# Optimization experiments

Hardware: AMD Instinct MI355X
Metric: run time of the kernel (lower is better)

Reference implementation:

```python
import jax, jax.numpy as jnp
import numpy as np

EPS = 1e-4

def mp_weight(w):
    # MP_GeoLinear eval-mode weight: normalize then scale by gain/sqrt(fan_in)
    w32 = w.astype(jnp.float32)
    norm = jnp.linalg.norm(w32, axis=1, keepdims=True)          # [out,1]
    fan_in = w.shape[1]
    denom = EPS + norm / np.sqrt(fan_in)                        # torch.add(eps, norm, alpha=sqrt(1/fan_in))
    wn = w32 / denom
    return (wn / np.sqrt(fan_in)).astype(w.dtype)               # gain=1


def setup_inputs() -> dict:
    key = jax.random.key(0)
    k1, k2, k3, k4 = jax.random.split(key, 4)
    N, E, C = 100000, 1600000, 128
    x = jax.random.normal(k1, (N, C), dtype=jnp.float32)
    edge_index = jax.random.randint(k2, (2, E), 0, N, dtype=jnp.int64)
    w_neigh = jax.random.normal(k3, (C, C), dtype=jnp.float32)
    w_res = jax.random.normal(k4, (C, C), dtype=jnp.float32)
    return {"x": x, "edge_index": edge_index, "w_neigh": w_neigh, "w_res": w_res}


def reference(x, edge_index, w_neigh, w_res):
    N = x.shape[0]
    row, col = edge_index[0], edge_index[1]            # source, target
    # degree of target nodes
    deg = jax.ops.segment_sum(jnp.ones_like(col, dtype=x.dtype), col, num_segments=N)
    deg_inv = jnp.where(deg > 0, deg ** -0.5, 0.0)     # inf -> 0
    norm = deg_inv[col]                                 # [E]
    # message: x_j * norm, aggregate: scatter-add into col
    msg = x[row] * norm[:, None]                        # [E,C]
    agg = jax.ops.segment_sum(msg, col, num_segments=N) # [N,C]
    neighbourhood = agg @ mp_weight(w_neigh).T
    residual = x @ mp_weight(w_res).T
    # mp_sum(residual, neighbourhood, t=0.5) = (a+b)/sqrt(2)
    join = (residual + neighbourhood) / np.sqrt(2.0)
    out = jnp.where((deg > 0)[:, None], join, residual)
    return out
```

## Files before the change

### kernel.cpp

```cpp
#include <hip/hip_runtime.h>
#include <hip/hip_bf16.h>

#define C 128
#define INV_SQRT2 0.7071067811865476f
#define NB 1024
#define BS 128
#define EPB 4096
#define NXCD 8
#define SUBCAP 384
#define LIDX_CAP 4096
#define AGS 68

typedef __attribute__((ext_vector_type(8))) short short8;
typedef __attribute__((ext_vector_type(4))) float f32x4;

__device__ inline ushort f2b(float f) {
    __hip_bfloat16 h = __float2bfloat16(f);
    return __builtin_bit_cast(ushort, h);
}


__global__ __launch_bounds__(512) void k_front(
    const int* __restrict__ row, const int* __restrict__ col, int E, int nblk,
    int* __restrict__ gcursor, unsigned int* __restrict__ recs,
    const float4* __restrict__ x, ushort* __restrict__ xb, int n4, int castBlocks,
    const float* __restrict__ w_res, const float* __restrict__ w_neigh,
    ushort* __restrict__ Bp)
{
    __shared__ int hist[NB];
    __shared__ int lbase[NB];
    int b = blockIdx.x;
    int t = threadIdx.x;
    if (b < nblk) {
        hist[t] = 0; hist[t + 512] = 0;
        __syncthreads();
        int base = b * EPB;
        #pragma unroll
        for (int i = 0; i < EPB / 512; i++) {
            int e = base + i * 512 + t;
            if (e < E) atomicAdd(&hist[col[e] >> 7], 1);
        }
        __syncthreads();
        int xcd = b & 7;
        int* gc = gcursor + xcd * NB;
        #pragma unroll
        for (int kx = 0; kx < 2; kx++) {
            int bb = t + kx * 512;
            int h = hist[bb];
            lbase[bb] = h ? atomicAdd(&gc[bb], h) : 0;
        }
        __syncthreads();
        hist[t] = 0; hist[t + 512] = 0;
        __syncthreads();
        #pragma unroll
        for (int i = 0; i < EPB / 512; i++) {
            int e = base + i * 512 + t;
            if (e < E) {
                int c = col[e];
                int kk = c >> 7;
                int p = atomicAdd(&hist[kk], 1) + lbase[kk];
                if (p < SUBCAP)
                    recs[((size_t)kk * NXCD + xcd) * SUBCAP + p] =
                        ((unsigned int)(c & 127) << 24) | (unsigned int)row[e];
            }
        }
    } else if (b < nblk + castBlocks) {
        int i = (b - nblk) * 512 + t;
        if (i < n4) {
            float4 v = x[i];
            ushort4 o;
            o.x = f2b(v.x); o.y = f2b(v.y); o.z = f2b(v.z); o.w = f2b(v.w);
            *(ushort4*)(xb + (size_t)i * 4) = o;
        }
        if (b == nblk && t < 32) {
            ushort4 z = make_ushort4(0, 0, 0, 0);
            *(ushort4*)(xb + ((size_t)n4 << 2) + (t << 2)) = z;
        }
    } else {
        int r = (b - nblk - castBlocks) * 8 + (t >> 6);
        int h = r >> 7;
        int i = r & 127;
        const float* w = h ? w_neigh : w_res;
        int lane = t & 63;
        float a = w[i * C + lane];
        float bb = w[i * C + lane + 64];
        float ss = a * a + bb * bb;
        #pragma unroll
        for (int off = 32; off > 0; off >>= 1) ss += __shfl_down(ss, off);
        ss = __shfl(ss, 0);
        float norm = sqrtf(ss);
        float denom = 1e-4f + norm * 0.08838834764831845f;
        float scale = 1.0f / (denom * 11.313708498984761f);
        int c1 = lane, c2 = lane + 64;
        Bp[(size_t)(h * 16 + (c1 >> 3)) * 1024 + i * 8 + (c1 & 7)] = f2b(a * scale);
        Bp[(size_t)(h * 16 + (c2 >> 3)) * 1024 + i * 8 + (c2 & 7)] = f2b(bb * scale);
    }
}


#define ACCUM(v) do { \
    acc[0] += __builtin_bit_cast(float, (v).x << 16); \
    acc[1] += __builtin_bit_cast(float, (v).x & 0xffff0000u); \
    acc[2] += __builtin_bit_cast(float, (v).y << 16); \
    acc[3] += __builtin_bit_cast(float, (v).y & 0xffff0000u); \
    acc[4] += __builtin_bit_cast(float, (v).z << 16); \
    acc[5] += __builtin_bit_cast(float, (v).z & 0xffff0000u); \
    acc[6] += __builtin_bit_cast(float, (v).w << 16); \
    acc[7] += __builtin_bit_cast(float, (v).w & 0xffff0000u); \
} while (0)

__global__ __launch_bounds__(512, 8) void k_fused(
    const unsigned int* __restrict__ recs, const int* __restrict__ gcursor,
    const ushort* __restrict__ xb, const ushort* __restrict__ Bp,
    int* __restrict__ lidxg, float* __restrict__ out, int N)
{
    __shared__ int shist[BS];
    __shared__ int sexcl[BS];
    __shared__ int scur[BS];
    __shared__ int scnt[NXCD];
    __shared__ uint sAgg[BS * AGS];

    int k = blockIdx.x;
    int t = threadIdx.x;
    const unsigned int* rb = recs + (size_t)k * NXCD * SUBCAP;
    int* lw = lidxg + (size_t)k * LIDX_CAP;

    if (t < NXCD) {
        int c = gcursor[t * NB + k];
        scnt[t] = (c > SUBCAP) ? SUBCAP : c;
    }
    if (t < BS) shist[t] = 0;
    __syncthreads();
    #pragma unroll 1
    for (int x = 0; x < NXCD; x++) {
        int cx = scnt[x];
        for (int i = t; i < cx; i += 512)
            atomicAdd(&shist[rb[x * SUBCAP + i] >> 24], 1);
    }
    __syncthreads();
    if (t < 64) {
        int a = shist[t], b = shist[t + 64];
        int pa = (a + 7) & ~7, pb = (b + 7) & ~7;
        int ia = pa, ib = pb;
        #pragma unroll
        for (int off = 1; off < 64; off <<= 1) {
            int ya = __shfl_up(ia, off);
            int yb = __shfl_up(ib, off);
            if (t >= off) { ia += ya; ib += yb; }
        }
        int tot0 = __shfl(ia, 63);
        int e0 = ia - pa;
        int e1 = ib - pb + tot0;
        sexcl[t] = e0;      scur[t] = e0;
        sexcl[t + 64] = e1; scur[t + 64] = e1;
    }
    __syncthreads();
    #pragma unroll 1
    for (int x = 0; x < NXCD; x++) {
        int cx = scnt[x];
        for (int i = t; i < cx; i += 512) {
            unsigned int r = rb[x * SUBCAP + i];
            int c = r >> 24;
            int p = atomicAdd(&scur[c], 1);
            lw[p] = (int)(r & 0xFFFFFF);
        }
    }
    if (t < BS) {
        int d = shist[t], b0 = sexcl[t];
        int pe = b0 + ((d + 7) & ~7);
        for (int p = b0 + d; p < pe; p++) lw[p] = N;
    }
    __syncthreads();

    int lane = t & 63;
    int wave = t >> 6;
    int s  = lane >> 4;
    int cl = lane & 15;
    const ushort* xcl = xb + (cl << 3);
    #pragma unroll 1
    for (int ln = wave * 16; ln < wave * 16 + 16; ln++) {
        int j  = sexcl[ln];
        int d  = shist[ln];
        int jend = j + ((d + 7) & ~7);
        float acc[8];
        #pragma unroll
        for (int i = 0; i < 8; i++) acc[i] = 0.f;
        for (; j + 16 <= jend; j += 16) {
            int i0 = lw[j + s];
            int i1 = lw[j + 4 + s];
            int i2 = lw[j + 8 + s];
            int i3 = lw[j + 12 + s];
            uint4 va = *(const uint4*)(xcl + ((size_t)i0 << 7));
            uint4 vb = *(const uint4*)(xcl + ((size_t)i1 << 7));
            uint4 vc = *(const uint4*)(xcl + ((size_t)i2 << 7));
            uint4 vd = *(const uint4*)(xcl + ((size_t)i3 << 7));
            ACCUM(va);
            ACCUM(vb);
            ACCUM(vc);
            ACCUM(vd);
        }
        if (j < jend) {
            int i0 = lw[j + s];
            int i1 = lw[j + 4 + s];
            uint4 va = *(const uint4*)(xcl + ((size_t)i0 << 7));
            uint4 vb = *(const uint4*)(xcl + ((size_t)i1 << 7));
            ACCUM(va);
            ACCUM(vb);
        }
        #pragma unroll
        for (int i = 0; i < 8; i++) {
            acc[i] += __shfl_xor(acc[i], 16);
            acc[i] += __shfl_xor(acc[i], 32);
        }
        float dd = (d > 0) ? rsqrtf((float)d) : 0.f;
        if (lane < 16) {
            uint4 o;
            o.x = (uint)f2b(acc[0] * dd) | ((uint)f2b(acc[1] * dd) << 16);
            o.y = (uint)f2b(acc[2] * dd) | ((uint)f2b(acc[3] * dd) << 16);
            o.z = (uint)f2b(acc[4] * dd) | ((uint)f2b(acc[5] * dd) << 16);
            o.w = (uint)f2b(acc[6] * dd) | ((uint)f2b(acc[7] * dd) << 16);
            *(uint4*)&sAgg[ln * AGS + cl * 4] = o;
        }
    }
    asm volatile("s_waitcnt lgkmcnt(0)" ::: "memory");

    int quad = lane >> 4;
    int l16  = lane & 15;
    long gbase = (long)k * BS;
    int arow = wave * 16 + l16;
    long garow = gbase + arow;
    if (garow >= N) garow = N - 1;

    f32x4 oacc[8];
    #pragma unroll
    for (int nt = 0; nt < 8; nt++) oacc[nt] = (f32x4){0.f, 0.f, 0.f, 0.f};

    #pragma unroll
    for (int kk = 0; kk < 8; kk++) {
        short8 af;
        if (kk < 4) {
            af = *(const short8*)(xb + garow * C + kk * 32 + quad * 8);
        } else {
            af = *(const short8*)&sAgg[arow * AGS + (kk - 4) * 16 + quad * 4];
        }
        #pragma unroll
        for (int nt = 0; nt < 8; nt++) {
            short8 bf = *(const short8*)(Bp +
                ((size_t)((kk * 4 + quad) * 128) + nt * 16 + l16) * 8);
            oacc[nt] = __builtin_amdgcn_mfma_f32_16x16x32_bf16(af, bf, oacc[nt], 0, 0, 0);
        }
    }

    #pragma unroll
    for (int r2 = 0; r2 < 4; r2++) {
        int rl = wave * 16 + quad * 4 + r2;
        long rowg = gbase + rl;
        if (rowg < N) {
            float sc = (shist[rl] > 0) ? INV_SQRT2 : 1.0f;
            float* o = out + rowg * C + l16;
            #pragma unroll
            for (int nt = 0; nt < 8; nt++)
                __builtin_nontemporal_store(oacc[nt][r2] * sc, &o[nt * 16]);
        }
    }
}


extern "C" void kernel_launch(void* const* d_in, const int* in_sizes, int n_in,
                              void* d_out, int out_size, void* d_ws, size_t ws_size,
                              hipStream_t stream) {
    const float* x       = (const float*)d_in[0];
    const int*   eidx    = (const int*)d_in[1];
    const float* w_neigh = (const float*)d_in[2];
    const float* w_res   = (const float*)d_in[3];
    float* out = (float*)d_out;

    int N = in_sizes[0] / C;
    int E = in_sizes[1] / 2;
    const int* row = eidx;
    const int* col = eidx + E;

    char* ws = (char*)d_ws;
    size_t off = 0;
    auto alloc = [&](size_t bytes) {
        size_t o = off;
        off += (bytes + 511) & ~(size_t)511;
        return o;
    };
    int nblk = (E + EPB - 1) / EPB;

    int*    gcursor    = (int*)(ws + alloc((size_t)NXCD * NB * 4));
    unsigned int* recs = (unsigned int*)(ws + alloc((size_t)NB * NXCD * SUBCAP * 4));
    ushort* Bp         = (ushort*)(ws + alloc((size_t)32 * 1024 * 2));
    ushort* xb         = (ushort*)(ws + alloc((size_t)N * C * 2 + 65536));
    int*    lidxg      = (int*)(ws + alloc((size_t)NB * LIDX_CAP * 4));
    (void)ws_size;

    hipMemsetAsync(gcursor, 0, (size_t)NXCD * NB * 4, stream);

    int nbuckets = (N + BS - 1) / BS;
    int n4 = N * C / 4;
    int castBlocks = (n4 + 511) / 512;

    k_front<<<nblk + castBlocks + 32, 512, 0, stream>>>(
        row, col, E, nblk, gcursor, recs,
        (const float4*)x, xb, n4, castBlocks, w_res, w_neigh, Bp);
    k_fused<<<nbuckets, 512, 0, stream>>>(recs, gcursor, xb, Bp, lidxg, out, N);
}
```

Before: 210.9 us.

## Merge front and fused kernels into one persistent cooperative kernel with grid sync

Replaces the two-kernel pipeline (bucketing/cast/weight prep, then aggregation+MFMA) with a single cooperative persistent kernel of up to 768 blocks. The blocks loop over the bucketing and weight work, cast x to bf16 through a dynamic atomic work counter, wait at a grid-wide barrier, then loop over the node buckets. This removes a kernel launch boundary and tail effects, but adds the grid sync cost and caps parallelism at the persistent grid size. It falls back to the old two-kernel path if the cooperative launch fails.

```diff
diff --git a/kernel.cpp b/kernel.cpp
--- a/kernel.cpp
+++ b/kernel.cpp
@@ -1,5 +1,8 @@
 #include <hip/hip_runtime.h>
 #include <hip/hip_bf16.h>
+#include <hip/hip_cooperative_groups.h>
+
+namespace cg = cooperative_groups;
 
 #define C 128
 #define INV_SQRT2 0.7071067811865476f
@@ -10,6 +13,7 @@
 #define SUBCAP 384
 #define LIDX_CAP 4096
 #define AGS 68
+#define COOP_GRID 768
 
 typedef __attribute__((ext_vector_type(8))) short short8;
 typedef __attribute__((ext_vector_type(4))) float f32x4;
@@ -17,6 +21,270 @@
 __device__ inline ushort f2b(float f) {
     __hip_bfloat16 h = __float2bfloat16(f);
     return __builtin_bit_cast(ushort, h);
+}
+
+#define ACCUM(v) do { \
+    acc[0] += __builtin_bit_cast(float, (v).x << 16); \
+    acc[1] += __builtin_bit_cast(float, (v).x & 0xffff0000u); \
+    acc[2] += __builtin_bit_cast(float, (v).y << 16); \
+    acc[3] += __builtin_bit_cast(float, (v).y & 0xffff0000u); \
+    acc[4] += __builtin_bit_cast(float, (v).z << 16); \
+    acc[5] += __builtin_bit_cast(float, (v).z & 0xffff0000u); \
+    acc[6] += __builtin_bit_cast(float, (v).w << 16); \
+    acc[7] += __builtin_bit_cast(float, (v).w & 0xffff0000u); \
+} while (0)
+
+
+__global__ __launch_bounds__(512, 8) void k_all(
+    const int* __restrict__ row, const int* __restrict__ col, int E, int nblk,
+    int* __restrict__ gcursor, unsigned int* __restrict__ recs,
+    const float4* __restrict__ x, ushort* __restrict__ xb, int n4,
+    int* __restrict__ castcur,
+    const float* __restrict__ w_res, const float* __restrict__ w_neigh,
+    ushort* __restrict__ Bp, int* __restrict__ lidxg,
+    float* __restrict__ out, int N)
+{
+    __shared__ uint sAgg[BS * AGS];
+    __shared__ int shist[BS];
+    __shared__ int sexcl[BS];
+    __shared__ int scur[BS];
+    __shared__ int scnt8[NXCD];
+    __shared__ int swork;
+
+    int b = blockIdx.x;
+    int t = threadIdx.x;
+    int gdim = gridDim.x;
+    int lane = t & 63;
+    int wave = t >> 6;
+    int nbuckets = (N + BS - 1) / BS;
+
+    for (int it = b; it < nblk + 32; it += gdim) {
+        __syncthreads();
+        if (it < nblk) {
+            int* hist  = (int*)sAgg;
+            int* lbase = (int*)sAgg + NB;
+            hist[t] = 0; hist[t + 512] = 0;
+            __syncthreads();
+            int base = it * EPB;
+            #pragma unroll
+            for (int i = 0; i < EPB / 512; i++) {
+                int e = base + i * 512 + t;
+                if (e < E) atomicAdd(&hist[col[e] >> 7], 1);
+            }
+            __syncthreads();
+            int xcd = it & 7;
+            int* gc = gcursor + xcd * NB;
+            #pragma unroll
+            for (int kx = 0; kx < 2; kx++) {
+                int bb = t + kx * 512;
+                int h = hist[bb];
+                lbase[bb] = h ? atomicAdd(&gc[bb], h) : 0;
+            }
+            __syncthreads();
+            hist[t] = 0; hist[t + 512] = 0;
+            __syncthreads();
+            #pragma unroll
+            for (int i = 0; i < EPB / 512; i++) {
+                int e = base + i * 512 + t;
+                if (e < E) {
+                    int c = col[e];
+                    int kk = c >> 7;
+                    int p = atomicAdd(&hist[kk], 1) + lbase[kk];
+                    if (p < SUBCAP)
+                        recs[((size_t)kk * NXCD + xcd) * SUBCAP + p] =
+                            ((unsigned int)(c & 127) << 24) | (unsigned int)row[e];
+                }
+            }
+        } else {
+            int r = (it - nblk) * 8 + wave;
+            int h = r >> 7;
+            int i = r & 127;
+            const float* w = h ? w_neigh : w_res;
+            float a = w[i * C + lane];
+            float bb = w[i * C + lane + 64];
+            float ss = a * a + bb * bb;
+            #pragma unroll
+            for (int off = 32; off > 0; off >>= 1) ss += __shfl_down(ss, off);
+            ss = __shfl(ss, 0);
+            float norm = sqrtf(ss);
+            float denom = 1e-4f + norm * 0.08838834764831845f;
+            float scale = 1.0f / (denom * 11.313708498984761f);
+            int c1 = lane, c2 = lane + 64;
+            Bp[(size_t)(h * 16 + (c1 >> 3)) * 1024 + i * 8 + (c1 & 7)] = f2b(a * scale);
+            Bp[(size_t)(h * 16 + (c2 >> 3)) * 1024 + i * 8 + (c2 & 7)] = f2b(bb * scale);
+        }
+    }
+    if (b == 0 && t < 32) {
+        ushort4 z = make_ushort4(0, 0, 0, 0);
+        *(ushort4*)(xb + ((size_t)n4 << 2) + (t << 2)) = z;
+    }
+
+    int nchunk = (n4 + 4095) >> 12;
+    for (;;) {
+        __syncthreads();
+        if (t == 0) swork = atomicAdd(castcur, 1);
+        __syncthreads();
+        int cc = swork;
+        if (cc >= nchunk) break;
+        int i0 = (cc << 12) + t;
+        #pragma unroll
+        for (int u = 0; u < 8; u++) {
+            int i = i0 + (u << 9);
+            if (i < n4) {
+                float4 v = x[i];
+                ushort4 o;
+                o.x = f2b(v.x); o.y = f2b(v.y); o.z = f2b(v.z); o.w = f2b(v.w);
+                *(ushort4*)(xb + (size_t)i * 4) = o;
+            }
+        }
+    }
+
+    __threadfence();
+    cg::this_grid().sync();
+    __threadfence();
+
+    for (int k = b; k < nbuckets; k += gdim) {
+        __syncthreads();
+        const unsigned int* rb = recs + (size_t)k * NXCD * SUBCAP;
+        int* lw = lidxg + (size_t)k * LIDX_CAP;
+
+        if (t < NXCD) {
+            int c0 = gcursor[t * NB + k];
+            scnt8[t] = (c0 > SUBCAP) ? SUBCAP : c0;
+        }
+        if (t < BS) shist[t] = 0;
+        __syncthreads();
+        #pragma unroll 1
+        for (int xx = 0; xx < NXCD; xx++) {
+            int cx = scnt8[xx];
+            for (int i = t; i < cx; i += 512)
+                atomicAdd(&shist[rb[xx * SUBCAP + i] >> 24], 1);
+        }
+        __syncthreads();
+        if (t < 64) {
+            int a = shist[t], bb = shist[t + 64];
+            int pa = (a + 7) & ~7, pb = (bb + 7) & ~7;
+            int ia = pa, ib = pb;
+            #pragma unroll
+            for (int off = 1; off < 64; off <<= 1) {
+                int ya = __shfl_up(ia, off);
+                int yb = __shfl_up(ib, off);
+                if (t >= off) { ia += ya; ib += yb; }
+            }
+            int tot0 = __shfl(ia, 63);
+            int e0 = ia - pa;
+            int e1 = ib - pb + tot0;
+            sexcl[t] = e0;      scur[t] = e0;
+            sexcl[t + 64] = e1; scur[t + 64] = e1;
+        }
+        __syncthreads();
+        #pragma unroll 1
+        for (int xx = 0; xx < NXCD; xx++) {
+            int cx = scnt8[xx];
+            for (int i = t; i < cx; i += 512) {
+                unsigned int r = rb[xx * SUBCAP + i];
+                int c = r >> 24;
+                int p = atomicAdd(&scur[c], 1);
+                lw[p] = (int)(r & 0xFFFFFF);
+            }
+        }
+        if (t < BS) {
+            int d = shist[t], b0 = sexcl[t];
+            int pe = b0 + ((d + 7) & ~7);
+            for (int p = b0 + d; p < pe; p++) lw[p] = N;
+        }
+        __syncthreads();
+
+        int s  = lane >> 4;
+        int cl = lane & 15;
+        const ushort* xcl = xb + (cl << 3);
+        #pragma unroll 1
+        for (int ln = wave * 16; ln < wave * 16 + 16; ln++) {
+            int j  = sexcl[ln];
+            int d  = shist[ln];
+            int jend = j + ((d + 7) & ~7);
+            float acc[8];
+            #pragma unroll
+            for (int i = 0; i < 8; i++) acc[i] = 0.f;
+            for (; j + 16 <= jend; j += 16) {
+                int i0 = lw[j + s];
+                int i1 = lw[j + 4 + s];
+                int i2 = lw[j + 8 + s];
+                int i3 = lw[j + 12 + s];
+                uint4 va = *(const uint4*)(xcl + ((size_t)i0 << 7));
+                uint4 vb = *(const uint4*)(xcl + ((size_t)i1 << 7));
+                uint4 vc = *(const uint4*)(xcl + ((size_t)i2 << 7));
+                uint4 vd = *(const uint4*)(xcl + ((size_t)i3 << 7));
+                ACCUM(va);
+                ACCUM(vb);
+                ACCUM(vc);
+                ACCUM(vd);
+            }
+            if (j < jend) {
+                int i0 = lw[j + s];
+                int i1 = lw[j + 4 + s];
+                uint4 va = *(const uint4*)(xcl + ((size_t)i0 << 7));
+                uint4 vb = *(const uint4*)(xcl + ((size_t)i1 << 7));
+                ACCUM(va);
+                ACCUM(vb);
+            }
+            #pragma unroll
+            for (int i = 0; i < 8; i++) {
+                acc[i] += __shfl_xor(acc[i], 16);
+                acc[i] += __shfl_xor(acc[i], 32);
+            }
+            float dd = (d > 0) ? rsqrtf((float)d) : 0.f;
+            if (lane < 16) {
+                uint4 o;
+                o.x = (uint)f2b(acc[0] * dd) | ((uint)f2b(acc[1] * dd) << 16);
+                o.y = (uint)f2b(acc[2] * dd) | ((uint)f2b(acc[3] * dd) << 16);
+                o.z = (uint)f2b(acc[4] * dd) | ((uint)f2b(acc[5] * dd) << 16);
+                o.w = (uint)f2b(acc[6] * dd) | ((uint)f2b(acc[7] * dd) << 16);
+                *(uint4*)&sAgg[ln * AGS + cl * 4] = o;
+            }
+        }
+        asm volatile("s_waitcnt lgkmcnt(0)" ::: "memory");
+
+        int quad = lane >> 4;
+        int l16  = lane & 15;
+        long gbase = (long)k * BS;
+        int arow = wave * 16 + l16;
+        long garow = gbase + arow;
+        if (garow >= N) garow = N - 1;
+
+        f32x4 oacc[8];
+        #pragma unroll
+        for (int nt = 0; nt < 8; nt++) oacc[nt] = (f32x4){0.f, 0.f, 0.f, 0.f};
+
+        #pragma unroll
+        for (int kk = 0; kk < 8; kk++) {
+            short8 af;
+            if (kk < 4) {
+                af = *(const short8*)(xb + garow * C + kk * 32 + quad * 8);
+            } else {
+                af = *(const short8*)&sAgg[arow * AGS + (kk - 4) * 16 + quad * 4];
+            }
+            #pragma unroll
+            for (int nt = 0; nt < 8; nt++) {
+                short8 bf = *(const short8*)(Bp +
+                    ((size_t)((kk * 4 + quad) * 128) + nt * 16 + l16) * 8);
+                oacc[nt] = __builtin_amdgcn_mfma_f32_16x16x32_bf16(af, bf, oacc[nt], 0, 0, 0);
+            }
+        }
+
+        #pragma unroll
+        for (int r2 = 0; r2 < 4; r2++) {
+            int rl = wave * 16 + quad * 4 + r2;
+            long rowg = gbase + rl;
+            if (rowg < N) {
+                float sc = (shist[rl] > 0) ? INV_SQRT2 : 1.0f;
+                float* o = out + rowg * C + l16;
+                #pragma unroll
+                for (int nt = 0; nt < 8; nt++)
+                    __builtin_nontemporal_store(oacc[nt][r2] * sc, &o[nt * 16]);
+            }
+        }
+    }
 }
 
 
@@ -97,18 +365,6 @@
     }
 }
 
-
-#define ACCUM(v) do { \
-    acc[0] += __builtin_bit_cast(float, (v).x << 16); \
-    acc[1] += __builtin_bit_cast(float, (v).x & 0xffff0000u); \
-    acc[2] += __builtin_bit_cast(float, (v).y << 16); \
-    acc[3] += __builtin_bit_cast(float, (v).y & 0xffff0000u); \
-    acc[4] += __builtin_bit_cast(float, (v).z << 16); \
-    acc[5] += __builtin_bit_cast(float, (v).z & 0xffff0000u); \
-    acc[6] += __builtin_bit_cast(float, (v).w << 16); \
-    acc[7] += __builtin_bit_cast(float, (v).w & 0xffff0000u); \
-} while (0)
-
 __global__ __launch_bounds__(512, 8) void k_fused(
     const unsigned int* __restrict__ recs, const int* __restrict__ gcursor,
     const ushort* __restrict__ xb, const ushort* __restrict__ Bp,
@@ -117,7 +373,7 @@
     __shared__ int shist[BS];
     __shared__ int sexcl[BS];
     __shared__ int scur[BS];
-    __shared__ int scnt[NXCD];
+    __shared__ int scnt8[NXCD];
     __shared__ uint sAgg[BS * AGS];
 
     int k = blockIdx.x;
@@ -126,21 +382,21 @@
     int* lw = lidxg + (size_t)k * LIDX_CAP;
 
     if (t < NXCD) {
-        int c = gcursor[t * NB + k];
-        scnt[t] = (c > SUBCAP) ? SUBCAP : c;
+        int c0 = gcursor[t * NB + k];
+        scnt8[t] = (c0 > SUBCAP) ? SUBCAP : c0;
     }
     if (t < BS) shist[t] = 0;
     __syncthreads();
     #pragma unroll 1
-    for (int x = 0; x < NXCD; x++) {
-        int cx = scnt[x];
+    for (int xx = 0; xx < NXCD; xx++) {
+        int cx = scnt8[xx];
         for (int i = t; i < cx; i += 512)
-            atomicAdd(&shist[rb[x * SUBCAP + i] >> 24], 1);
+            atomicAdd(&shist[rb[xx * SUBCAP + i] >> 24], 1);
     }
     __syncthreads();
     if (t < 64) {
-        int a = shist[t], b = shist[t + 64];
-        int pa = (a + 7) & ~7, pb = (b + 7) & ~7;
+        int a = shist[t], bb = shist[t + 64];
+        int pa = (a + 7) & ~7, pb = (bb + 7) & ~7;
         int ia = pa, ib = pb;
         #pragma unroll
         for (int off = 1; off < 64; off <<= 1) {
@@ -156,10 +412,10 @@
     }
     __syncthreads();
     #pragma unroll 1
-    for (int x = 0; x < NXCD; x++) {
-        int cx = scnt[x];
+    for (int xx = 0; xx < NXCD; xx++) {
+        int cx = scnt8[xx];
         for (int i = t; i < cx; i += 512) {
-            unsigned int r = rb[x * SUBCAP + i];
+            unsigned int r = rb[xx * SUBCAP + i];
             int c = r >> 24;
             int p = atomicAdd(&scur[c], 1);
             lw[p] = (int)(r & 0xFFFFFF);
@@ -289,21 +545,36 @@
     };
     int nblk = (E + EPB - 1) / EPB;
 
-    int*    gcursor    = (int*)(ws + alloc((size_t)NXCD * NB * 4));
+    int*    gcursor    = (int*)(ws + alloc((size_t)(NXCD * NB + 128) * 4));
     unsigned int* recs = (unsigned int*)(ws + alloc((size_t)NB * NXCD * SUBCAP * 4));
     ushort* Bp         = (ushort*)(ws + alloc((size_t)32 * 1024 * 2));
     ushort* xb         = (ushort*)(ws + alloc((size_t)N * C * 2 + 65536));
     int*    lidxg      = (int*)(ws + alloc((size_t)NB * LIDX_CAP * 4));
+    int*    castcur    = gcursor + NXCD * NB;
     (void)ws_size;
 
-    hipMemsetAsync(gcursor, 0, (size_t)NXCD * NB * 4, stream);
+    hipMemsetAsync(gcursor, 0, (size_t)(NXCD * NB + 128) * 4, stream);
 
     int nbuckets = (N + BS - 1) / BS;
     int n4 = N * C / 4;
-    int castBlocks = (n4 + 511) / 512;
-
-    k_front<<<nblk + castBlocks + 32, 512, 0, stream>>>(
-        row, col, E, nblk, gcursor, recs,
-        (const float4*)x, xb, n4, castBlocks, w_res, w_neigh, Bp);
-    k_fused<<<nbuckets, 512, 0, stream>>>(recs, gcursor, xb, Bp, lidxg, out, N);
+
+    int grid = nbuckets < COOP_GRID ? (nbuckets & ~7) : COOP_GRID;
+    if (grid < 8) grid = 8;
+
+    const float4* x4 = (const float4*)x;
+    void* args[] = {
+        (void*)&row, (void*)&col, (void*)&E, (void*)&nblk,
+        (void*)&gcursor, (void*)&recs, (void*)&x4, (void*)&xb, (void*)&n4,
+        (void*)&castcur, (void*)&w_res, (void*)&w_neigh,
+        (void*)&Bp, (void*)&lidxg, (void*)&out, (void*)&N
+    };
+    hipError_t rc = hipLaunchCooperativeKernel((const void*)k_all, dim3(grid),
+                                               dim3(512), args, 0, stream);
+    if (rc != hipSuccess) {
+        int castBlocks = (n4 + 511) / 512;
+        k_front<<<nblk + castBlocks + 32, 512, 0, stream>>>(
+            row, col, E, nblk, gcursor, recs,
+            x4, xb, n4, castBlocks, w_res, w_neigh, Bp);
+        k_fused<<<nbuckets, 512, 0, stream>>>(recs, gcursor, xb, Bp, lidxg, out, N);
+    }
 }
```

Result: slower. 752.9 us (+257.1%).
